# Kernel optimization log

Hardware: AMD Instinct MI355X
Metric: run time of the kernel (lower is better)

Reference implementation:

```python
import jax, jax.numpy as jnp
import numpy as np

B, T, D = 2, 1024, 1024
H = 8            # num_heads
DK = 128         # head_k_dim
DV = 128         # head_v_dim
M = 128          # num_slots (== head_k_dim by default)
K = 32           # topk
EPS = 1e-5
SCALE = 1.0


def _rmsnorm(x, w, eps=EPS):
    return x * jax.lax.rsqrt(jnp.mean(x * x, axis=-1, keepdims=True) + eps) * w


def setup_inputs() -> dict:
    key = jax.random.key(0)
    ks = jax.random.split(key, 12)
    def lin(k, fan_in, fan_out):
        return jax.random.normal(k, (fan_in, fan_out), jnp.float32) / np.sqrt(fan_in).astype(np.float32)
    hidden_states = jax.random.normal(ks[0], (B, T, D), jnp.float32)
    Wq = lin(ks[1], D, H * DK)
    Wk = lin(ks[2], D, H * DK)
    Wv = lin(ks[3], D, H * DV)
    Wr = lin(ks[4], D, H * M)
    Wa = lin(ks[5], D, H)
    # Mamba2-style decay params
    A_log = jnp.log(jax.random.uniform(ks[6], (H,), jnp.float32, 1e-3, 16.0))
    dt = jnp.exp(jax.random.uniform(ks[7], (H,), jnp.float32) * (np.log(0.1) - np.log(0.001)) + np.log(0.001))
    dt = jnp.clip(dt, 1e-4, None)
    dt_bias = dt + jnp.log(-jnp.expm1(-dt))
    q_norm_w = jnp.ones((DK,), jnp.float32) + 0.01 * jax.random.normal(ks[8], (DK,), jnp.float32)
    k_norm_w = jnp.ones((DK,), jnp.float32) + 0.01 * jax.random.normal(ks[9], (DK,), jnp.float32)
    g_norm_w = jnp.ones((D,), jnp.float32) + 0.01 * jax.random.normal(ks[10], (D,), jnp.float32)
    Wo = lin(ks[11], H * DV, D)
    return dict(hidden_states=hidden_states, Wq=Wq, Wk=Wk, Wv=Wv, Wr=Wr, Wa=Wa,
                A_log=A_log, dt_bias=dt_bias, q_norm_w=q_norm_w, k_norm_w=k_norm_w,
                g_norm_w=g_norm_w, Wo=Wo)


def reference(hidden_states, Wq, Wk, Wv, Wr, Wa, A_log, dt_bias, q_norm_w, k_norm_w, g_norm_w, Wo):
    b, t, d = hidden_states.shape
    # projections
    q = (hidden_states @ Wq).reshape(b, t, H, DK)
    k = (hidden_states @ Wk).reshape(b, t, H, DK)
    v = jax.nn.silu((hidden_states @ Wv).reshape(b, t, H, DV))
    router = (hidden_states @ Wr).reshape(b, t, H, M)
    # Mamba2 decay (log-space, per head)
    f_head = -jnp.exp(A_log) * jax.nn.softplus(hidden_states @ Wa + dt_bias)  # [b,t,H]
    # swish feature map + per-head RMSNorm
    q = _rmsnorm(jax.nn.silu(q), q_norm_w)
    k = _rmsnorm(jax.nn.silu(k), k_norm_w)
    # sigmoid router scores, top-k slot routing (eval: no gumbel noise)
    scores = jax.nn.sigmoid(router)                    # [b,t,H,M]
    top_w, top_i = jax.lax.top_k(scores, K)            # [b,t,H,K]
    top_w = top_w / (jnp.sum(top_w, axis=-1, keepdims=True) + 1e-9)
    n = b * t * H
    rows = jnp.arange(n)[:, None]
    s_multihot = jnp.zeros((n, M), scores.dtype).at[rows, top_i.reshape(n, K)].set(
        top_w.reshape(n, K)).reshape(b, t, H, M)
    f = f_head[..., None] * s_multihot                 # [b,t,H,M], log decay per slot
    s = 1.0 - jnp.exp(f)                               # write gate per slot
    # decayed linear-attention recurrence over slots (M == DK):
    #   S_t[i,j] = exp(f_t[i]) * S_{t-1}[i,j] + s_t[i]*k_t[i]*v_t[j]
    #   o_t[j]   = scale * sum_i q_t[i] * S_t[i,j]
    def step(S, xs):
        q_t, k_t, v_t, f_t, s_t = xs                   # [b,H,*]
        S = jnp.exp(f_t)[..., None] * S + (s_t * k_t)[..., None] * v_t[..., None, :]
        o_t = jnp.einsum('bhk,bhkv->bhv', q_t, S) * SCALE
        return S, o_t
    xs = tuple(jnp.swapaxes(a, 0, 1) for a in (q, k, v, f, s))  # time-major
    S0 = jnp.zeros((b, H, DK, DV), q.dtype)
    _, o = jax.lax.scan(step, S0, xs)                  # o: [t,b,H,DV]
    o = jnp.swapaxes(o, 0, 1).reshape(b, t, H * DV)
    o = _rmsnorm(o, g_norm_w)                          # g_norm over hidden_size
    return o @ Wo
```

## Files before the change

kernel.cpp:

```cpp
#include <hip/hip_runtime.h>
#include <stdint.h>
#include <stddef.h>

#define H_ 8
#define T_ 1024

typedef __attribute__((ext_vector_type(8))) short s16x8;
typedef __attribute__((ext_vector_type(4))) float f32x4;
typedef __attribute__((ext_vector_type(16))) float f32x16;

static __device__ __forceinline__ unsigned short f2bf(float f){
  unsigned u = __float_as_uint(f);
  u += 0x7fffu + ((u >> 16) & 1u);
  return (unsigned short)(u >> 16);
}
static __device__ __forceinline__ float bf2f(unsigned short b){
  return __uint_as_float(((unsigned)b) << 16);
}
static __device__ __forceinline__ unsigned int pack_hl(float x){
  unsigned short h = f2bf(x);
  unsigned short l = f2bf(x - bf2f(h));
  return ((unsigned int)h << 16) | l;
}
static __device__ __forceinline__ void gl_lds16(const unsigned short* g, unsigned short* l){
  __builtin_amdgcn_global_load_lds((const __attribute__((address_space(1))) unsigned int*)g,
                                   (__attribute__((address_space(3))) unsigned int*)l,
                                   16, 0, 0);
}

__global__ void cast_hs(const float* __restrict__ X, unsigned short* __restrict__ hi,
                        unsigned short* __restrict__ lo){
  size_t idx = ((size_t)blockIdx.x * 256 + threadIdx.x) * 8;
  float4 a = *(const float4*)(X + idx);
  float4 b = *(const float4*)(X + idx + 4);
  float v[8] = {a.x,a.y,a.z,a.w,b.x,b.y,b.z,b.w};
  unsigned short hh[8], ll[8];
#pragma unroll
  for(int i=0;i<8;i++){ hh[i]=f2bf(v[i]); ll[i]=f2bf(v[i]-bf2f(hh[i])); }
  ushort4 h0,h1,l0,l1;
  h0.x=hh[0];h0.y=hh[1];h0.z=hh[2];h0.w=hh[3];
  h1.x=hh[4];h1.y=hh[5];h1.z=hh[6];h1.w=hh[7];
  l0.x=ll[0];l0.y=ll[1];l0.z=ll[2];l0.w=ll[3];
  l1.x=ll[4];l1.y=ll[5];l1.z=ll[6];l1.w=ll[7];
  *(ushort4*)&hi[idx]=h0; *(ushort4*)&hi[idx+4]=h1;
  *(ushort4*)&lo[idx]=l0; *(ushort4*)&lo[idx+4]=l1;
}

__global__ void wtrans(const float* __restrict__ Wq, const float* __restrict__ Wk,
                       const float* __restrict__ Wv, const float* __restrict__ Wr,
                       const float* __restrict__ Wo,
                       unsigned short* __restrict__ WcatT3, unsigned short* __restrict__ WrThi,
                       unsigned short* __restrict__ WrTlo, unsigned short* __restrict__ WoT){
  __shared__ float tile[32][33];
  int z = blockIdx.z;
  const float* src = (z==0)?Wq:(z==1)?Wk:(z==2)?Wv:(z==3)?Wr:Wo;
  int c0 = blockIdx.x*32;
  int k0 = blockIdx.y*32;
  int tx = threadIdx.x, ty = threadIdx.y;
#pragma unroll
  for(int r=0;r<32;r+=8)
    tile[ty+r][tx] = src[(size_t)(k0+ty+r)*1024 + c0 + tx];
  __syncthreads();
#pragma unroll
  for(int r=0;r<32;r+=8){
    int c = c0 + ty + r;
    int k = k0 + tx;
    float v = tile[tx][ty+r];
    if(z < 3){
      WcatT3[((size_t)(z*1024 + c))*1024 + k] = f2bf(v);
    } else if(z == 3){
      unsigned short hv = f2bf(v);
      WrThi[(size_t)c*1024 + k] = hv;
      WrTlo[(size_t)c*1024 + k] = f2bf(v - bf2f(hv));
    } else {
      WoT[(size_t)c*1024 + k] = f2bf(v);
    }
  }
}

__launch_bounds__(256)
__global__ void gemm_fused(const unsigned short* __restrict__ Xhi, const unsigned short* __restrict__ Xlo,
                           const unsigned short* __restrict__ WcatT3, const unsigned short* __restrict__ WrThi,
                           const unsigned short* __restrict__ WrTlo,
                           float* __restrict__ C1, float* __restrict__ R){
  __shared__ unsigned short As[128*32];
  __shared__ unsigned short Bs[128*32];
  int blk = blockIdx.x;
  bool router = (blk >= 384);
  int bx, by, N, nseg;
  float* Cout;
  if(!router){ bx = blk%24; by = blk/24; N = 3072; nseg = 1; Cout = C1; }
  else { int rb = blk-384; bx = rb%8; by = rb/8; N = 1024; nseg = 3; Cout = R; }
  int tid = threadIdx.x;
  int mBase = by*128, nBase = bx*128;
  int w = tid>>6, lane = tid&63, wr = w>>1, wc = w&1;
  int kg = lane>>4, l15 = lane&15;
  f32x4 acc[4][4];
#pragma unroll
  for(int i=0;i<4;i++)
#pragma unroll
    for(int j=0;j<4;j++) acc[i][j] = (f32x4){0.f,0.f,0.f,0.f};
  size_t aoff = (size_t)(mBase + (tid>>2))*1024 + (tid&3)*8;
  size_t boff = (size_t)(nBase + (tid>>2))*1024 + (tid&3)*8;
  for(int s=0; s<3; s++){
    if(s >= nseg) break;
    const unsigned short* Ap = (s==2) ? Xlo : Xhi;
    const unsigned short* Bp = router ? ((s==1) ? WrTlo : WrThi) : WcatT3;
    const unsigned short* gA = Ap + aoff;
    const unsigned short* gB = Bp + boff;
    for(int kb=0; kb<1024; kb+=32){
      gl_lds16(gA + kb,                    &As[tid*8]);
      gl_lds16(gA + (size_t)64*1024 + kb,  &As[2048 + tid*8]);
      gl_lds16(gB + kb,                    &Bs[tid*8]);
      gl_lds16(gB + (size_t)64*1024 + kb,  &Bs[2048 + tid*8]);
      __syncthreads();
      s16x8 afr[4], bfr[4];
#pragma unroll
      for(int f=0;f<4;f++){
        afr[f] = *(const s16x8*)&As[(wr*64 + f*16 + l15)*32 + kg*8];
        bfr[f] = *(const s16x8*)&Bs[(wc*64 + f*16 + l15)*32 + kg*8];
      }
#pragma unroll
      for(int fm=0;fm<4;fm++)
#pragma unroll
        for(int fn=0;fn<4;fn++)
          acc[fm][fn] = __builtin_amdgcn_mfma_f32_16x16x32_bf16(afr[fm], bfr[fn], acc[fm][fn], 0,0,0);
      __syncthreads();
    }
  }
#pragma unroll
  for(int fm=0;fm<4;fm++)
#pragma unroll
    for(int fn=0;fn<4;fn++){
      int col = nBase + wc*64 + fn*16 + l15;
      int row = mBase + wr*64 + fm*16 + kg*4;
#pragma unroll
      for(int r=0;r<4;r++) Cout[(size_t)(row+r)*N + col] = acc[fm][fn][r];
    }
}

__launch_bounds__(256)
__global__ void gemm_bf16(const unsigned short* __restrict__ A,
                          const unsigned short* __restrict__ BT,
                          float* __restrict__ C, int M, int N, int K){
  __shared__ unsigned short As[128*32];
  __shared__ unsigned short Bs[128*32];
  int tid = threadIdx.x;
  int mBase = blockIdx.y*128, nBase = blockIdx.x*128;
  int w = tid>>6, lane = tid&63, wr = w>>1, wc = w&1;
  int kg = lane>>4, l15 = lane&15;
  f32x4 acc[4][4];
#pragma unroll
  for(int i=0;i<4;i++)
#pragma unroll
    for(int j=0;j<4;j++) acc[i][j] = (f32x4){0.f,0.f,0.f,0.f};
  const unsigned short* gA = A + (size_t)(mBase + (tid>>2))*K + (tid&3)*8;
  const unsigned short* gB = BT + (size_t)(nBase + (tid>>2))*K + (tid&3)*8;
  for(int kb=0; kb<K; kb+=32){
    gl_lds16(gA + kb,                 &As[tid*8]);
    gl_lds16(gA + (size_t)64*K + kb,  &As[2048 + tid*8]);
    gl_lds16(gB + kb,                 &Bs[tid*8]);
    gl_lds16(gB + (size_t)64*K + kb,  &Bs[2048 + tid*8]);
    __syncthreads();
    s16x8 afr[4], bfr[4];
#pragma unroll
    for(int f=0;f<4;f++){
      afr[f] = *(const s16x8*)&As[(wr*64 + f*16 + l15)*32 + kg*8];
      bfr[f] = *(const s16x8*)&Bs[(wc*64 + f*16 + l15)*32 + kg*8];
    }
#pragma unroll
    for(int fm=0;fm<4;fm++)
#pragma unroll
      for(int fn=0;fn<4;fn++)
        acc[fm][fn] = __builtin_amdgcn_mfma_f32_16x16x32_bf16(afr[fm], bfr[fn], acc[fm][fn], 0,0,0);
    __syncthreads();
  }
#pragma unroll
  for(int fm=0;fm<4;fm++)
#pragma unroll
    for(int fn=0;fn<4;fn++){
      int col = nBase + wc*64 + fn*16 + l15;
      int row = mBase + wr*64 + fm*16 + kg*4;
#pragma unroll
      for(int r=0;r<4;r++) C[(size_t)(row+r)*N + col] = acc[fm][fn][r];
    }
}

__global__ void fhead_k(const float* __restrict__ X, const float* __restrict__ Wa,
                        const float* __restrict__ A_log, const float* __restrict__ dtb,
                        float* __restrict__ fh){
  __shared__ float xs[1024];
  int n = blockIdx.x, tid = threadIdx.x;
  *(float4*)&xs[tid*4] = *(const float4*)&X[(size_t)n*1024 + tid*4];
  __syncthreads();
  int h = tid>>5, l = tid&31;
  float s = 0.f;
  for(int k=l;k<1024;k+=32) s += xs[k]*Wa[(size_t)k*8 + h];
  s += __shfl_xor(s,1); s += __shfl_xor(s,2); s += __shfl_xor(s,4);
  s += __shfl_xor(s,8); s += __shfl_xor(s,16);
  if(l==0){
    float z = s + dtb[h];
    float sp = (z > 20.f) ? z : log1pf(expf(z));
    fh[(size_t)n*8 + h] = -expf(A_log[h]) * sp;
  }
}

__launch_bounds__(128)
__global__ void postproc(const float* __restrict__ C1, const float* __restrict__ R,
                         const float* __restrict__ fh, const float* __restrict__ qw,
                         const float* __restrict__ kw,
                         float* __restrict__ Qd, float* __restrict__ Wt,
                         float* __restrict__ Fd, float* __restrict__ Vd){
  __shared__ float sc[128];
  __shared__ float red[2];
  int blk = blockIdx.x;
  int n = blk>>3, h = blk&7;
  int i = threadIdx.x;
  int b = n>>10, t = n&1023;
  size_t base = ((size_t)(b*H_ + h)*T_ + t)*128 + i;
  size_t cb = (size_t)n*3072;
  float qraw = C1[cb + h*128 + i];
  float kraw = C1[cb + 1024 + h*128 + i];
  float vraw = C1[cb + 2048 + h*128 + i];
  float rlog = R[(size_t)n*1024 + h*128 + i];
  float qs = qraw/(1.f+expf(-qraw));
  float ks = kraw/(1.f+expf(-kraw));
  float vv = vraw/(1.f+expf(-vraw));
  float si = 1.f/(1.f+expf(-rlog));
  sc[i] = si;
  __syncthreads();
  int cnt = 0;
#pragma unroll 8
  for(int j4=0;j4<128;j4+=4){
    float4 s4 = *(const float4*)&sc[j4];
    cnt += (s4.x>si) || (s4.x==si && (j4+0)<i);
    cnt += (s4.y>si) || (s4.y==si && (j4+1)<i);
    cnt += (s4.z>si) || (s4.z==si && (j4+2)<i);
    cnt += (s4.w>si) || (s4.w==si && (j4+3)<i);
  }
  bool sel = cnt < 32;
  float x;
  x = qs*qs;
  x+=__shfl_xor(x,1);x+=__shfl_xor(x,2);x+=__shfl_xor(x,4);x+=__shfl_xor(x,8);x+=__shfl_xor(x,16);x+=__shfl_xor(x,32);
  __syncthreads(); if((i&63)==0) red[i>>6]=x; __syncthreads();
  float qn = qs * rsqrtf((red[0]+red[1])/128.f + 1e-5f) * qw[i];
  x = ks*ks;
  x+=__shfl_xor(x,1);x+=__shfl_xor(x,2);x+=__shfl_xor(x,4);x+=__shfl_xor(x,8);x+=__shfl_xor(x,16);x+=__shfl_xor(x,32);
  __syncthreads(); if((i&63)==0) red[i>>6]=x; __syncthreads();
  float kn = ks * rsqrtf((red[0]+red[1])/128.f + 1e-5f) * kw[i];
  x = sel ? si : 0.f;
  x+=__shfl_xor(x,1);x+=__shfl_xor(x,2);x+=__shfl_xor(x,4);x+=__shfl_xor(x,8);x+=__shfl_xor(x,16);x+=__shfl_xor(x,32);
  __syncthreads(); if((i&63)==0) red[i>>6]=x; __syncthreads();
  float wsum = red[0]+red[1];
  float wgt = sel ? si/(wsum + 1e-9f) : 0.f;
  float f = fh[(size_t)n*8 + h] * wgt;
  Qd[base] = qn;
  Wt[base] = (1.f - expf(f)) * kn;
  Fd[base] = f;
  Vd[base] = vv;
}

__launch_bounds__(256)
__global__ void chunk_sum(float* __restrict__ Fd, const float* __restrict__ Wt,
                          const float* __restrict__ Vd, float* __restrict__ dS,
                          float* __restrict__ E){
  __shared__ float Fc[32][132];
  __shared__ float Kh[32][132];
  int blk = blockIdx.x, bh = blk>>5, c = blk&31;
  int tid = threadIdx.x;
  int w = tid>>6, lane = tid&63;
  size_t fbase = ((size_t)bh*T_ + (size_t)c*32)*128;
#pragma unroll
  for(int v=0; v<4; v++){
    int e = v*1024 + tid*4;
    int t2 = e>>7, i0 = e&127;
    float4 f4 = *(const float4*)&Fd[fbase + e];
    *(float4*)&Fc[t2][i0] = f4;
  }
  __syncthreads();
  if(tid < 128){
    float a = 0.f;
    for(int t2=0;t2<32;t2++){ a += Fc[t2][tid]; Fc[t2][tid] = a; }
  }
  __syncthreads();
#pragma unroll
  for(int v=0; v<4; v++){
    int e = v*1024 + tid*4;
    int t2 = e>>7, i0 = e&127;
    float4 fc4 = *(const float4*)&Fc[t2][i0];
    *(float4*)&Fd[fbase + e] = fc4;
    float4 ft  = *(const float4*)&Fc[31][i0];
    float4 w4  = *(const float4*)&Wt[fbase + e];
    float4 kh;
    kh.x = w4.x * expf(ft.x - fc4.x);
    kh.y = w4.y * expf(ft.y - fc4.y);
    kh.z = w4.z * expf(ft.z - fc4.z);
    kh.w = w4.w * expf(ft.w - fc4.w);
    *(float4*)&Kh[t2][i0] = kh;
  }
  if(tid < 128) E[((size_t)bh*32 + c)*128 + tid] = expf(Fc[31][tid]);
  __syncthreads();
  int ig = lane>>3, jg = lane&7;
  const float* Vp = Vd + fbase;
  f32x4 acc[4][4];
#pragma unroll
  for(int a=0;a<4;a++)
#pragma unroll
    for(int q=0;q<4;q++) acc[a][q] = (f32x4){0.f,0.f,0.f,0.f};
#pragma unroll 4
  for(int t2=0;t2<32;t2++){
    float4 kq = *(const float4*)&Kh[t2][w*32 + ig*4];
    float4 v0 = *(const float4*)&Vp[t2*128 + jg*4];
    float4 v1 = *(const float4*)&Vp[t2*128 + jg*4 + 32];
    float4 v2 = *(const float4*)&Vp[t2*128 + jg*4 + 64];
    float4 v3 = *(const float4*)&Vp[t2*128 + jg*4 + 96];
    float kk[4] = {kq.x,kq.y,kq.z,kq.w};
#pragma unroll
    for(int a=0;a<4;a++){
      acc[a][0] += kk[a]*(f32x4){v0.x,v0.y,v0.z,v0.w};
      acc[a][1] += kk[a]*(f32x4){v1.x,v1.y,v1.z,v1.w};
      acc[a][2] += kk[a]*(f32x4){v2.x,v2.y,v2.z,v2.w};
      acc[a][3] += kk[a]*(f32x4){v3.x,v3.y,v3.z,v3.w};
    }
  }
  size_t dbase = (size_t)blk*16384;
#pragma unroll
  for(int q=0;q<4;q++)
#pragma unroll
    for(int jj=0;jj<4;jj++){
      float4 o4 = make_float4(acc[0][q][jj],acc[1][q][jj],acc[2][q][jj],acc[3][q][jj]);
      *(float4*)&dS[dbase + (size_t)(jg*4 + 32*q + jj)*128 + w*32 + ig*4] = o4;
    }
}

__global__ void scan_k(float* __restrict__ dS, const float* __restrict__ E){
  int g = blockIdx.x*256 + threadIdx.x;
  int bh = g>>12;
  int e4 = (g&4095)*4;
  int i0 = e4 & 127;
  float4 S = make_float4(0.f,0.f,0.f,0.f);
  for(int c=0;c<32;c++){
    size_t off = ((size_t)(bh*32 + c))*16384 + e4;
    float4 d   = *(const float4*)&dS[off];
    float4 Ec  = *(const float4*)&E[((size_t)(bh*32 + c))*128 + i0];
    *(float4*)&dS[off] = S;
    S.x = Ec.x*S.x + d.x;
    S.y = Ec.y*S.y + d.y;
    S.z = Ec.z*S.z + d.z;
    S.w = Ec.w*S.w + d.w;
  }
}

__launch_bounds__(256)
__global__ void chunk_out(const float* __restrict__ Qd, const float* __restrict__ Wt,
                          const float* __restrict__ Fd, const float* __restrict__ Vd,
                          const float* __restrict__ ST, float* __restrict__ O){
  __shared__ unsigned int qtP[32][132];
  __shared__ unsigned int ktP[32][132];
  __shared__ unsigned int Vt[128][36];
  __shared__ float Amat[32][40];
  int blk = blockIdx.x, bh = blk>>5, c = blk&31;
  int b = bh>>3, h = bh&7;
  int tid = threadIdx.x, w = tid>>6, lane = tid&63;
  int m = lane&31, hi = lane>>5;
  size_t fbase = ((size_t)bh*T_ + (size_t)c*32)*128;
#pragma unroll
  for(int p=0;p<4;p++){
    int e = p*1024 + tid*4;
    int t2 = e>>7, i0 = e&127;
    float4 f4 = *(const float4*)&Fd[fbase + e];
    float4 q4 = *(const float4*)&Qd[fbase + e];
    float4 w4 = *(const float4*)&Wt[fbase + e];
    float fv[4] = {f4.x,f4.y,f4.z,f4.w};
    float qv[4] = {q4.x,q4.y,q4.z,q4.w};
    float wv[4] = {w4.x,w4.y,w4.z,w4.w};
    uint4 qp, kp;
    unsigned int qa[4], ka[4];
#pragma unroll
    for(int j=0;j<4;j++){
      float ef = expf(fv[j]);
      qa[j] = pack_hl(qv[j]*ef);
      ka[j] = pack_hl(wv[j]/ef);
    }
    qp.x=qa[0]; qp.y=qa[1]; qp.z=qa[2]; qp.w=qa[3];
    kp.x=ka[0]; kp.y=ka[1]; kp.z=ka[2]; kp.w=ka[3];
    *(uint4*)&qtP[t2][i0] = qp;
    *(uint4*)&ktP[t2][i0] = kp;
  }
  {
    int n = tid&127, th = (tid>>7)*16;
    unsigned int vp[16];
#pragma unroll
    for(int j=0;j<16;j++) vp[j] = pack_hl(Vd[fbase + (size_t)(th+j)*128 + n]);
#pragma unroll
    for(int j=0;j<16;j+=4){
      uint4 v4; v4.x=vp[j]; v4.y=vp[j+1]; v4.z=vp[j+2]; v4.w=vp[j+3];
      *(uint4*)&Vt[n][th+j] = v4;
    }
  }
  __syncthreads();
  if(w == 0){
    f32x16 am;
#pragma unroll
    for(int r=0;r<16;r++) am[r] = 0.f;
#pragma unroll
    for(int s=0;s<8;s++){
      int ko = s*16 + hi*8;
      uint4 qa = *(const uint4*)&qtP[m][ko];
      uint4 qb = *(const uint4*)&qtP[m][ko+4];
      uint4 ka = *(const uint4*)&ktP[m][ko];
      uint4 kb = *(const uint4*)&ktP[m][ko+4];
      s16x8 qh, ql, kh, kl;
      unsigned int qw_[8] = {qa.x,qa.y,qa.z,qa.w,qb.x,qb.y,qb.z,qb.w};
      unsigned int kw_[8] = {ka.x,ka.y,ka.z,ka.w,kb.x,kb.y,kb.z,kb.w};
#pragma unroll
      for(int j=0;j<8;j++){
        qh[j]=(short)(qw_[j]>>16); ql[j]=(short)(qw_[j]&0xffff);
        kh[j]=(short)(kw_[j]>>16); kl[j]=(short)(kw_[j]&0xffff);
      }
      am = __builtin_amdgcn_mfma_f32_32x32x16_bf16(qh, kh, am, 0,0,0);
      am = __builtin_amdgcn_mfma_f32_32x32x16_bf16(qh, kl, am, 0,0,0);
      am = __builtin_amdgcn_mfma_f32_32x32x16_bf16(ql, kh, am, 0,0,0);
    }
#pragma unroll
    for(int r=0;r<16;r++){
      int rm = (r&3) + 8*(r>>2) + 4*hi;
      Amat[rm][m] = (m <= rm) ? am[r] : 0.f;
    }
  }
  f32x16 oacc;
#pragma unroll
  for(int r=0;r<16;r++) oacc[r] = 0.f;
  const float* Sp = ST + (size_t)blk*16384 + (size_t)(w*32 + m)*128;
#pragma unroll
  for(int s=0;s<8;s++){
    int ko = s*16 + hi*8;
    uint4 qa = *(const uint4*)&qtP[m][ko];
    uint4 qb = *(const uint4*)&qtP[m][ko+4];
    s16x8 qh, ql;
    unsigned int qw_[8] = {qa.x,qa.y,qa.z,qa.w,qb.x,qb.y,qb.z,qb.w};
#pragma unroll
    for(int j=0;j<8;j++){ qh[j]=(short)(qw_[j]>>16); ql[j]=(short)(qw_[j]&0xffff); }
    float4 s0 = *(const float4*)&Sp[ko];
    float4 s1 = *(const float4*)&Sp[ko+4];
    float sv[8] = {s0.x,s0.y,s0.z,s0.w,s1.x,s1.y,s1.z,s1.w};
    s16x8 sh, sl;
#pragma unroll
    for(int j=0;j<8;j++){
      unsigned short hh = f2bf(sv[j]);
      sh[j] = (short)hh; sl[j] = (short)f2bf(sv[j]-bf2f(hh));
    }
    oacc = __builtin_amdgcn_mfma_f32_32x32x16_bf16(qh, sh, oacc, 0,0,0);
    oacc = __builtin_amdgcn_mfma_f32_32x32x16_bf16(qh, sl, oacc, 0,0,0);
    oacc = __builtin_amdgcn_mfma_f32_32x32x16_bf16(ql, sh, oacc, 0,0,0);
  }
  __syncthreads();
#pragma unroll
  for(int s=0;s<2;s++){
    int uo = s*16 + hi*8;
    float4 a0 = *(const float4*)&Amat[m][uo];
    float4 a1 = *(const float4*)&Amat[m][uo+4];
    float av[8] = {a0.x,a0.y,a0.z,a0.w,a1.x,a1.y,a1.z,a1.w};
    s16x8 ah, al;
#pragma unroll
    for(int j=0;j<8;j++){
      unsigned short hh = f2bf(av[j]);
      ah[j] = (short)hh; al[j] = (short)f2bf(av[j]-bf2f(hh));
    }
    uint4 v0 = *(const uint4*)&Vt[w*32 + m][uo];
    uint4 v1 = *(const uint4*)&Vt[w*32 + m][uo+4];
    unsigned int vw[8] = {v0.x,v0.y,v0.z,v0.w,v1.x,v1.y,v1.z,v1.w};
    s16x8 vh, vl;
#pragma unroll
    for(int j=0;j<8;j++){ vh[j]=(short)(vw[j]>>16); vl[j]=(short)(vw[j]&0xffff); }
    oacc = __builtin_amdgcn_mfma_f32_32x32x16_bf16(ah, vh, oacc, 0,0,0);
    oacc = __builtin_amdgcn_mfma_f32_32x32x16_bf16(ah, vl, oacc, 0,0,0);
    oacc = __builtin_amdgcn_mfma_f32_32x32x16_bf16(al, vh, oacc, 0,0,0);
  }
#pragma unroll
  for(int r=0;r<16;r++){
    int tok = (r&3) + 8*(r>>2) + 4*hi;
    O[((size_t)(b*T_ + c*32 + tok))*1024 + h*128 + w*32 + m] = oacc[r];
  }
}

__global__ void gnorm_k(const float* __restrict__ Ob, const float* __restrict__ gw,
                        unsigned short* __restrict__ On){
  __shared__ float red[4];
  int n = blockIdx.x, tid = threadIdx.x;
  size_t base = (size_t)n*1024 + tid*4;
  float4 x = *(const float4*)&Ob[base];
  float ss = x.x*x.x + x.y*x.y + x.z*x.z + x.w*x.w;
  ss+=__shfl_xor(ss,1);ss+=__shfl_xor(ss,2);ss+=__shfl_xor(ss,4);
  ss+=__shfl_xor(ss,8);ss+=__shfl_xor(ss,16);ss+=__shfl_xor(ss,32);
  if((tid&63)==0) red[tid>>6]=ss;
  __syncthreads();
  float sc = rsqrtf((red[0]+red[1]+red[2]+red[3])/1024.f + 1e-5f);
  float4 g = *(const float4*)&gw[tid*4];
  ushort4 o4;
  o4.x=f2bf(x.x*sc*g.x); o4.y=f2bf(x.y*sc*g.y);
  o4.z=f2bf(x.z*sc*g.z); o4.w=f2bf(x.w*sc*g.w);
  *(ushort4*)&On[base]=o4;
}

extern "C" void kernel_launch(void* const* d_in, const int* in_sizes, int n_in,
                              void* d_out, int out_size, void* d_ws, size_t ws_size,
                              hipStream_t stream){
  const float* hs   = (const float*)d_in[0];
  const float* Wq   = (const float*)d_in[1];
  const float* Wk   = (const float*)d_in[2];
  const float* Wv   = (const float*)d_in[3];
  const float* Wr   = (const float*)d_in[4];
  const float* Wa   = (const float*)d_in[5];
  const float* A_log= (const float*)d_in[6];
  const float* dtb  = (const float*)d_in[7];
  const float* qw   = (const float*)d_in[8];
  const float* kw   = (const float*)d_in[9];
  const float* gw   = (const float*)d_in[10];
  const float* Wo   = (const float*)d_in[11];
  float* out = (float*)d_out;

  char* wsp = (char*)d_ws;
  size_t off = 0;
  auto alloc = [&](size_t bytes)->void*{ void* p = wsp + off; off += (bytes + 255) & ~(size_t)255; return p; };
  unsigned short* Xhi    = (unsigned short*)alloc(2048ull*1024*2);
  unsigned short* Xlo    = (unsigned short*)alloc(2048ull*1024*2);
  unsigned short* WcatT3 = (unsigned short*)alloc(3072ull*1024*2);
  unsigned short* WrThi  = (unsigned short*)alloc(1024ull*1024*2);
  unsigned short* WrTlo  = (unsigned short*)alloc(1024ull*1024*2);
  unsigned short* WoT    = (unsigned short*)alloc(1024ull*1024*2);
  float* C1 = (float*)alloc(2048ull*3072*4);
  float* R  = (float*)alloc(2048ull*1024*4);
  float* fh = (float*)alloc(2048ull*8*4);
  float* Qd = (float*)alloc(16ull*1024*128*4);
  float* Wt = (float*)alloc(16ull*1024*128*4);
  float* Fd = (float*)alloc(16ull*1024*128*4);
  float* Vd = (float*)alloc(16ull*1024*128*4);
  float* E  = (float*)alloc(16ull*32*128*4);
  float* dS = (float*)alloc(16ull*32*16384*4);
  float* Ob = (float*)alloc(2048ull*1024*4);
  unsigned short* On = (unsigned short*)alloc(2048ull*1024*2);
  (void)ws_size; (void)in_sizes; (void)n_in; (void)out_size;

  cast_hs    <<<dim3(1024),        dim3(256),   0, stream>>>(hs, Xhi, Xlo);
  wtrans     <<<dim3(32,32,5),     dim3(32,8),  0, stream>>>(Wq,Wk,Wv,Wr,Wo, WcatT3,WrThi,WrTlo,WoT);
  gemm_fused <<<dim3(512),         dim3(256),   0, stream>>>(Xhi, Xlo, WcatT3, WrThi, WrTlo, C1, R);
  fhead_k    <<<dim3(2048),        dim3(256),   0, stream>>>(hs, Wa, A_log, dtb, fh);
  postproc   <<<dim3(16384),       dim3(128),   0, stream>>>(C1, R, fh, qw, kw, Qd, Wt, Fd, Vd);
  chunk_sum  <<<dim3(512),         dim3(256),   0, stream>>>(Fd, Wt, Vd, dS, E);
  scan_k     <<<dim3(256),         dim3(256),   0, stream>>>(dS, E);
  chunk_out  <<<dim3(512),         dim3(256),   0, stream>>>(Qd, Wt, Fd, Vd, dS, Ob);
  gnorm_k    <<<dim3(2048),        dim3(256),   0, stream>>>(Ob, gw, On);
  gemm_bf16  <<<dim3(8,16),        dim3(256),   0, stream>>>(On, WoT, out, 2048, 1024, 1024);
}
```

Baseline: 297.8 us.

## Fuse cast with decay head, split router GEMM segments, swizzle LDS, retile output GEMM

Merges the hidden-state bf16 split cast with the per-head decay projection into one kernel. The router GEMM's three hi/lo passes become separate blocks that write partial sums into a reused scratch buffer, and postproc adds them. This evens out block work and adds XCD-aware block remapping. Both GEMMs get an XOR-swizzled LDS layout to avoid bank conflicts, and the output GEMM uses 128x64 tiles to launch more blocks. Top-k ranking switches to packed 64-bit key compares, and the scan runs scalar per thread with more blocks. In exchange the router partials add extra memory traffic.

```diff
diff --git a/kernel.cpp b/kernel.cpp
--- a/kernel.cpp
+++ b/kernel.cpp
@@ -28,22 +28,35 @@
                                    16, 0, 0);
 }
 
-__global__ void cast_hs(const float* __restrict__ X, unsigned short* __restrict__ hi,
-                        unsigned short* __restrict__ lo){
-  size_t idx = ((size_t)blockIdx.x * 256 + threadIdx.x) * 8;
-  float4 a = *(const float4*)(X + idx);
-  float4 b = *(const float4*)(X + idx + 4);
-  float v[8] = {a.x,a.y,a.z,a.w,b.x,b.y,b.z,b.w};
-  unsigned short hh[8], ll[8];
-#pragma unroll
-  for(int i=0;i<8;i++){ hh[i]=f2bf(v[i]); ll[i]=f2bf(v[i]-bf2f(hh[i])); }
-  ushort4 h0,h1,l0,l1;
-  h0.x=hh[0];h0.y=hh[1];h0.z=hh[2];h0.w=hh[3];
-  h1.x=hh[4];h1.y=hh[5];h1.z=hh[6];h1.w=hh[7];
-  l0.x=ll[0];l0.y=ll[1];l0.z=ll[2];l0.w=ll[3];
-  l1.x=ll[4];l1.y=ll[5];l1.z=ll[6];l1.w=ll[7];
-  *(ushort4*)&hi[idx]=h0; *(ushort4*)&hi[idx+4]=h1;
-  *(ushort4*)&lo[idx]=l0; *(ushort4*)&lo[idx+4]=l1;
+__global__ void prep_k(const float* __restrict__ X, const float* __restrict__ Wa,
+                       const float* __restrict__ A_log, const float* __restrict__ dtb,
+                       unsigned short* __restrict__ hi, unsigned short* __restrict__ lo,
+                       float* __restrict__ fh){
+  __shared__ float xs[1024];
+  int n = blockIdx.x, tid = threadIdx.x;
+  size_t base = (size_t)n*1024 + tid*4;
+  float4 x = *(const float4*)&X[base];
+  *(float4*)&xs[tid*4] = x;
+  float v[4] = {x.x,x.y,x.z,x.w};
+  ushort4 h4, l4;
+  unsigned short hh[4], ll[4];
+#pragma unroll
+  for(int j=0;j<4;j++){ hh[j]=f2bf(v[j]); ll[j]=f2bf(v[j]-bf2f(hh[j])); }
+  h4.x=hh[0];h4.y=hh[1];h4.z=hh[2];h4.w=hh[3];
+  l4.x=ll[0];l4.y=ll[1];l4.z=ll[2];l4.w=ll[3];
+  *(ushort4*)&hi[base] = h4;
+  *(ushort4*)&lo[base] = l4;
+  __syncthreads();
+  int h = tid>>5, l = tid&31;
+  float s = 0.f;
+  for(int k=l;k<1024;k+=32) s += xs[k]*Wa[(size_t)k*8 + h];
+  s += __shfl_xor(s,1); s += __shfl_xor(s,2); s += __shfl_xor(s,4);
+  s += __shfl_xor(s,8); s += __shfl_xor(s,16);
+  if(l==0){
+    float z = s + dtb[h];
+    float sp = (z > 20.f) ? z : log1pf(expf(z));
+    fh[(size_t)n*8 + h] = -expf(A_log[h]) * sp;
+  }
 }
 
 __global__ void wtrans(const float* __restrict__ Wq, const float* __restrict__ Wk,
@@ -82,15 +95,25 @@
 __global__ void gemm_fused(const unsigned short* __restrict__ Xhi, const unsigned short* __restrict__ Xlo,
                            const unsigned short* __restrict__ WcatT3, const unsigned short* __restrict__ WrThi,
                            const unsigned short* __restrict__ WrTlo,
-                           float* __restrict__ C1, float* __restrict__ R){
+                           float* __restrict__ C1, float* __restrict__ Rp){
   __shared__ unsigned short As[128*32];
   __shared__ unsigned short Bs[128*32];
-  int blk = blockIdx.x;
-  bool router = (blk >= 384);
-  int bx, by, N, nseg;
+  int bid = blockIdx.x;
+  int blk = (bid&7)*96 + (bid>>3);
+  const unsigned short *Ap, *Bp;
   float* Cout;
-  if(!router){ bx = blk%24; by = blk/24; N = 3072; nseg = 1; Cout = C1; }
-  else { int rb = blk-384; bx = rb%8; by = rb/8; N = 1024; nseg = 3; Cout = R; }
+  int bx, by, N;
+  if(blk < 384){
+    bx = blk%24; by = blk/24; N = 3072;
+    Ap = Xhi; Bp = WcatT3; Cout = C1;
+  } else {
+    int rb = blk-384;
+    int seg = rb>>7, t = rb&127;
+    bx = t&7; by = t>>3; N = 1024;
+    Ap = (seg==2) ? Xlo : Xhi;
+    Bp = (seg==1) ? WrTlo : WrThi;
+    Cout = Rp + (size_t)seg*2048*1024;
+  }
   int tid = threadIdx.x;
   int mBase = by*128, nBase = bx*128;
   int w = tid>>6, lane = tid&63, wr = w>>1, wc = w&1;
@@ -100,33 +123,29 @@
   for(int i=0;i<4;i++)
 #pragma unroll
     for(int j=0;j<4;j++) acc[i][j] = (f32x4){0.f,0.f,0.f,0.f};
-  size_t aoff = (size_t)(mBase + (tid>>2))*1024 + (tid&3)*8;
-  size_t boff = (size_t)(nBase + (tid>>2))*1024 + (tid&3)*8;
-  for(int s=0; s<3; s++){
-    if(s >= nseg) break;
-    const unsigned short* Ap = (s==2) ? Xlo : Xhi;
-    const unsigned short* Bp = router ? ((s==1) ? WrTlo : WrThi) : WcatT3;
-    const unsigned short* gA = Ap + aoff;
-    const unsigned short* gB = Bp + boff;
-    for(int kb=0; kb<1024; kb+=32){
-      gl_lds16(gA + kb,                    &As[tid*8]);
-      gl_lds16(gA + (size_t)64*1024 + kb,  &As[2048 + tid*8]);
-      gl_lds16(gB + kb,                    &Bs[tid*8]);
-      gl_lds16(gB + (size_t)64*1024 + kb,  &Bs[2048 + tid*8]);
-      __syncthreads();
-      s16x8 afr[4], bfr[4];
-#pragma unroll
-      for(int f=0;f<4;f++){
-        afr[f] = *(const s16x8*)&As[(wr*64 + f*16 + l15)*32 + kg*8];
-        bfr[f] = *(const s16x8*)&Bs[(wc*64 + f*16 + l15)*32 + kg*8];
-      }
-#pragma unroll
-      for(int fm=0;fm<4;fm++)
-#pragma unroll
-        for(int fn=0;fn<4;fn++)
-          acc[fm][fn] = __builtin_amdgcn_mfma_f32_16x16x32_bf16(afr[fm], bfr[fn], acc[fm][fn], 0,0,0);
-      __syncthreads();
-    }
+  int srow = tid>>2, scc = (tid&3) ^ ((srow>>1)&3);
+  const unsigned short* gA = Ap + (size_t)(mBase + srow)*1024 + scc*8;
+  const unsigned short* gB = Bp + (size_t)(nBase + srow)*1024 + scc*8;
+  for(int kb=0; kb<1024; kb+=32){
+    gl_lds16(gA + kb,                    &As[tid*8]);
+    gl_lds16(gA + (size_t)64*1024 + kb,  &As[2048 + tid*8]);
+    gl_lds16(gB + kb,                    &Bs[tid*8]);
+    gl_lds16(gB + (size_t)64*1024 + kb,  &Bs[2048 + tid*8]);
+    __syncthreads();
+    s16x8 afr[4], bfr[4];
+#pragma unroll
+    for(int f=0;f<4;f++){
+      int r = f*16 + l15;
+      int xr = (kg ^ ((r>>1)&3))*8;
+      afr[f] = *(const s16x8*)&As[(wr*64 + r)*32 + xr];
+      bfr[f] = *(const s16x8*)&Bs[(wc*64 + r)*32 + xr];
+    }
+#pragma unroll
+    for(int fm=0;fm<4;fm++)
+#pragma unroll
+      for(int fn=0;fn<4;fn++)
+        acc[fm][fn] = __builtin_amdgcn_mfma_f32_16x16x32_bf16(afr[fm], bfr[fn], acc[fm][fn], 0,0,0);
+    __syncthreads();
   }
 #pragma unroll
   for(int fm=0;fm<4;fm++)
@@ -140,78 +159,66 @@
 }
 
 __launch_bounds__(256)
-__global__ void gemm_bf16(const unsigned short* __restrict__ A,
-                          const unsigned short* __restrict__ BT,
-                          float* __restrict__ C, int M, int N, int K){
+__global__ void gemm_out(const unsigned short* __restrict__ A,
+                         const unsigned short* __restrict__ BT,
+                         float* __restrict__ C){
   __shared__ unsigned short As[128*32];
-  __shared__ unsigned short Bs[128*32];
+  __shared__ unsigned short Bs[64*32];
+  const int K = 1024, N = 1024;
   int tid = threadIdx.x;
-  int mBase = blockIdx.y*128, nBase = blockIdx.x*128;
-  int w = tid>>6, lane = tid&63, wr = w>>1, wc = w&1;
+  int mBase = blockIdx.y*128, nBase = blockIdx.x*64;
+  int w = tid>>6, lane = tid&63;
+  int mh = w>>1, nh = w&1;
   int kg = lane>>4, l15 = lane&15;
-  f32x4 acc[4][4];
+  f32x4 acc[4][2];
 #pragma unroll
   for(int i=0;i<4;i++)
 #pragma unroll
-    for(int j=0;j<4;j++) acc[i][j] = (f32x4){0.f,0.f,0.f,0.f};
-  const unsigned short* gA = A + (size_t)(mBase + (tid>>2))*K + (tid&3)*8;
-  const unsigned short* gB = BT + (size_t)(nBase + (tid>>2))*K + (tid&3)*8;
+    for(int j=0;j<2;j++) acc[i][j] = (f32x4){0.f,0.f,0.f,0.f};
+  int srow = tid>>2, scc = (tid&3) ^ ((srow>>1)&3);
+  const unsigned short* gA = A  + (size_t)(mBase + srow)*K + scc*8;
+  const unsigned short* gB = BT + (size_t)(nBase + srow)*K + scc*8;
   for(int kb=0; kb<K; kb+=32){
-    gl_lds16(gA + kb,                 &As[tid*8]);
-    gl_lds16(gA + (size_t)64*K + kb,  &As[2048 + tid*8]);
-    gl_lds16(gB + kb,                 &Bs[tid*8]);
-    gl_lds16(gB + (size_t)64*K + kb,  &Bs[2048 + tid*8]);
+    gl_lds16(gA + kb,              &As[tid*8]);
+    gl_lds16(gA + (size_t)64*K + kb, &As[2048 + tid*8]);
+    gl_lds16(gB + kb,              &Bs[tid*8]);
     __syncthreads();
-    s16x8 afr[4], bfr[4];
+    s16x8 afr[4], bfr[2];
 #pragma unroll
     for(int f=0;f<4;f++){
-      afr[f] = *(const s16x8*)&As[(wr*64 + f*16 + l15)*32 + kg*8];
-      bfr[f] = *(const s16x8*)&Bs[(wc*64 + f*16 + l15)*32 + kg*8];
+      int r = f*16 + l15;
+      afr[f] = *(const s16x8*)&As[(mh*64 + r)*32 + (kg ^ ((r>>1)&3))*8];
+    }
+#pragma unroll
+    for(int f=0;f<2;f++){
+      int r = f*16 + l15;
+      bfr[f] = *(const s16x8*)&Bs[(nh*32 + r)*32 + (kg ^ ((r>>1)&3))*8];
     }
 #pragma unroll
     for(int fm=0;fm<4;fm++)
 #pragma unroll
-      for(int fn=0;fn<4;fn++)
+      for(int fn=0;fn<2;fn++)
         acc[fm][fn] = __builtin_amdgcn_mfma_f32_16x16x32_bf16(afr[fm], bfr[fn], acc[fm][fn], 0,0,0);
     __syncthreads();
   }
 #pragma unroll
   for(int fm=0;fm<4;fm++)
 #pragma unroll
-    for(int fn=0;fn<4;fn++){
-      int col = nBase + wc*64 + fn*16 + l15;
-      int row = mBase + wr*64 + fm*16 + kg*4;
+    for(int fn=0;fn<2;fn++){
+      int col = nBase + nh*32 + fn*16 + l15;
+      int row = mBase + mh*64 + fm*16 + kg*4;
 #pragma unroll
       for(int r=0;r<4;r++) C[(size_t)(row+r)*N + col] = acc[fm][fn][r];
     }
 }
 
-__global__ void fhead_k(const float* __restrict__ X, const float* __restrict__ Wa,
-                        const float* __restrict__ A_log, const float* __restrict__ dtb,
-                        float* __restrict__ fh){
-  __shared__ float xs[1024];
-  int n = blockIdx.x, tid = threadIdx.x;
-  *(float4*)&xs[tid*4] = *(const float4*)&X[(size_t)n*1024 + tid*4];
-  __syncthreads();
-  int h = tid>>5, l = tid&31;
-  float s = 0.f;
-  for(int k=l;k<1024;k+=32) s += xs[k]*Wa[(size_t)k*8 + h];
-  s += __shfl_xor(s,1); s += __shfl_xor(s,2); s += __shfl_xor(s,4);
-  s += __shfl_xor(s,8); s += __shfl_xor(s,16);
-  if(l==0){
-    float z = s + dtb[h];
-    float sp = (z > 20.f) ? z : log1pf(expf(z));
-    fh[(size_t)n*8 + h] = -expf(A_log[h]) * sp;
-  }
-}
-
 __launch_bounds__(128)
-__global__ void postproc(const float* __restrict__ C1, const float* __restrict__ R,
+__global__ void postproc(const float* __restrict__ C1, const float* __restrict__ Rp,
                          const float* __restrict__ fh, const float* __restrict__ qw,
                          const float* __restrict__ kw,
                          float* __restrict__ Qd, float* __restrict__ Wt,
                          float* __restrict__ Fd, float* __restrict__ Vd){
-  __shared__ float sc[128];
+  __shared__ unsigned long long keys[128];
   __shared__ float red[2];
   int blk = blockIdx.x;
   int n = blk>>3, h = blk&7;
@@ -219,24 +226,24 @@
   int b = n>>10, t = n&1023;
   size_t base = ((size_t)(b*H_ + h)*T_ + t)*128 + i;
   size_t cb = (size_t)n*3072;
+  size_t rb = (size_t)n*1024 + h*128 + i;
   float qraw = C1[cb + h*128 + i];
   float kraw = C1[cb + 1024 + h*128 + i];
   float vraw = C1[cb + 2048 + h*128 + i];
-  float rlog = R[(size_t)n*1024 + h*128 + i];
+  float rlog = Rp[rb] + Rp[2048ull*1024 + rb] + Rp[2ull*2048*1024 + rb];
   float qs = qraw/(1.f+expf(-qraw));
   float ks = kraw/(1.f+expf(-kraw));
   float vv = vraw/(1.f+expf(-vraw));
   float si = 1.f/(1.f+expf(-rlog));
-  sc[i] = si;
+  unsigned long long ki = (((unsigned long long)__float_as_uint(si)) << 7) | (unsigned)(127 - i);
+  keys[i] = ki;
   __syncthreads();
   int cnt = 0;
 #pragma unroll 8
-  for(int j4=0;j4<128;j4+=4){
-    float4 s4 = *(const float4*)&sc[j4];
-    cnt += (s4.x>si) || (s4.x==si && (j4+0)<i);
-    cnt += (s4.y>si) || (s4.y==si && (j4+1)<i);
-    cnt += (s4.z>si) || (s4.z==si && (j4+2)<i);
-    cnt += (s4.w>si) || (s4.w==si && (j4+3)<i);
+  for(int j=0;j<128;j+=2){
+    ulonglong2 k2 = *(const ulonglong2*)&keys[j];
+    cnt += (k2.x > ki);
+    cnt += (k2.y > ki);
   }
   bool sel = cnt < 32;
   float x;
@@ -335,19 +342,15 @@
 
 __global__ void scan_k(float* __restrict__ dS, const float* __restrict__ E){
   int g = blockIdx.x*256 + threadIdx.x;
-  int bh = g>>12;
-  int e4 = (g&4095)*4;
-  int i0 = e4 & 127;
-  float4 S = make_float4(0.f,0.f,0.f,0.f);
+  int bh = g>>14, e = g&16383;
+  int i = e&127;
+  float S = 0.f;
   for(int c=0;c<32;c++){
-    size_t off = ((size_t)(bh*32 + c))*16384 + e4;
-    float4 d   = *(const float4*)&dS[off];
-    float4 Ec  = *(const float4*)&E[((size_t)(bh*32 + c))*128 + i0];
-    *(float4*)&dS[off] = S;
-    S.x = Ec.x*S.x + d.x;
-    S.y = Ec.y*S.y + d.y;
-    S.z = Ec.z*S.z + d.z;
-    S.w = Ec.w*S.w + d.w;
+    size_t off = ((size_t)(bh*32 + c))*16384 + e;
+    float d  = dS[off];
+    float Ec = E[((size_t)(bh*32 + c))*128 + i];
+    dS[off] = S;
+    S = Ec*S + d;
   }
 }
 
@@ -530,7 +533,6 @@
   unsigned short* WrTlo  = (unsigned short*)alloc(1024ull*1024*2);
   unsigned short* WoT    = (unsigned short*)alloc(1024ull*1024*2);
   float* C1 = (float*)alloc(2048ull*3072*4);
-  float* R  = (float*)alloc(2048ull*1024*4);
   float* fh = (float*)alloc(2048ull*8*4);
   float* Qd = (float*)alloc(16ull*1024*128*4);
   float* Wt = (float*)alloc(16ull*1024*128*4);
@@ -540,16 +542,16 @@
   float* dS = (float*)alloc(16ull*32*16384*4);
   float* Ob = (float*)alloc(2048ull*1024*4);
   unsigned short* On = (unsigned short*)alloc(2048ull*1024*2);
+  float* Rp = dS;
   (void)ws_size; (void)in_sizes; (void)n_in; (void)out_size;
 
-  cast_hs    <<<dim3(1024),        dim3(256),   0, stream>>>(hs, Xhi, Xlo);
+  prep_k     <<<dim3(2048),        dim3(256),   0, stream>>>(hs, Wa, A_log, dtb, Xhi, Xlo, fh);
   wtrans     <<<dim3(32,32,5),     dim3(32,8),  0, stream>>>(Wq,Wk,Wv,Wr,Wo, WcatT3,WrThi,WrTlo,WoT);
-  gemm_fused <<<dim3(512),         dim3(256),   0, stream>>>(Xhi, Xlo, WcatT3, WrThi, WrTlo, C1, R);
-  fhead_k    <<<dim3(2048),        dim3(256),   0, stream>>>(hs, Wa, A_log, dtb, fh);
-  postproc   <<<dim3(16384),       dim3(128),   0, stream>>>(C1, R, fh, qw, kw, Qd, Wt, Fd, Vd);
+  gemm_fused <<<dim3(768),         dim3(256),   0, stream>>>(Xhi, Xlo, WcatT3, WrThi, WrTlo, C1, Rp);
+  postproc   <<<dim3(16384),       dim3(128),   0, stream>>>(C1, Rp, fh, qw, kw, Qd, Wt, Fd, Vd);
   chunk_sum  <<<dim3(512),         dim3(256),   0, stream>>>(Fd, Wt, Vd, dS, E);
-  scan_k     <<<dim3(256),         dim3(256),   0, stream>>>(dS, E);
+  scan_k     <<<dim3(1024),        dim3(256),   0, stream>>>(dS, E);
   chunk_out  <<<dim3(512),         dim3(256),   0, stream>>>(Qd, Wt, Fd, Vd, dS, Ob);
   gnorm_k    <<<dim3(2048),        dim3(256),   0, stream>>>(Ob, gw, On);
-  gemm_bf16  <<<dim3(8,16),        dim3(256),   0, stream>>>(On, WoT, out, 2048, 1024, 1024);
-}
+  gemm_out   <<<dim3(16,16),       dim3(256),   0, stream>>>(On, WoT, out);
+}
```

Measured after the change: 264.2 us. 1.13x faster.
